# Kernel tuning notes

Hardware: AMD Instinct MI355X
Metric: run time of the kernel (lower is better)

Reference implementation:

```python
import jax, jax.numpy as jnp
import numpy as np

NHID = 512
T_K, T_Q, B = 256, 128, 8


def setup_inputs() -> dict:
    key = jax.random.key(0)
    k1, k2, k3, k4, k5 = jax.random.split(key, 5)
    query = jax.random.normal(k1, (T_Q, B, NHID), dtype=jnp.float32)
    c_key = jax.random.normal(k2, (T_K, B, NHID), dtype=jnp.float32)
    mask = jax.random.randint(k3, (T_K, B), 0, 2).astype(bool)
    # att_mlp params: Linear(2*nhid, nhid) -> Tanh -> Linear(nhid, 1)
    # stored as [in, out] so y = x @ W + b (torch Linear weight transposed)
    W1 = jax.random.normal(k4, (2 * NHID, NHID), dtype=jnp.float32) / np.sqrt(2 * NHID)
    b1 = jnp.zeros((NHID,), dtype=jnp.float32)
    W2 = jax.random.normal(k5, (NHID, 1), dtype=jnp.float32) / np.sqrt(NHID)
    b2 = jnp.zeros((1,), dtype=jnp.float32)
    return {"query": query, "c_key": c_key, "mask": mask,
            "W1": W1, "b1": b1, "W2": W2, "b2": b2}


def reference(query, c_key, mask, W1, b1, W2, b2):
    H = query.shape[-1]
    # cat([k_expand, q_expand], -1) @ W1 == k @ W1[:H] + q @ W1[H:]
    # (avoids materializing the [T_k, T_q, B, 2H] concat the torch code builds)
    k_proj = jnp.einsum('kbh,hd->kbd', c_key, W1[:H])   # [T_k, B, H]
    q_proj = jnp.einsum('qbh,hd->qbd', query, W1[H:])   # [T_q, B, H]
    h = jnp.tanh(k_proj[:, None, :, :] + q_proj[None, :, :, :] + b1)  # [T_k, T_q, B, H]
    att_score = jnp.einsum('kqbh,ho->kqb', h, W2) + b2[0]             # [T_k, T_q, B]
    att_score = jnp.where(mask[:, None, :], -jnp.inf, att_score)
    att_prob = jax.nn.softmax(att_score, axis=0)                      # softmax over keys
    # c_val defaults to c_key in the original forward
    ant_vec = jnp.einsum('kqb,kbh->qbh', att_prob, c_key)             # [T_q, B, H]
    return ant_vec, att_prob
```

## Files before the change

### kernel.cpp

```cpp
#include <hip/hip_runtime.h>
#include <math.h>

#define NHID 512
#define T_K  256
#define T_Q  128
#define BB   8

constexpr float C2L2E = 2.8853900817779268f;
constexpr float L2E   = 1.4426950408889634f;

__device__ __forceinline__ float fexp2(float x) { return __builtin_amdgcn_exp2f(x); }
__device__ __forceinline__ float frcp(float x)  { return __builtin_amdgcn_rcpf(x); }

typedef __attribute__((ext_vector_type(8))) short bf16x8;
typedef __attribute__((ext_vector_type(4))) float f32x4;

__device__ __forceinline__ unsigned short f2bf(float x) {
    unsigned u = __builtin_bit_cast(unsigned, x);
    unsigned r = (u + 0x7FFFu + ((u >> 16) & 1u)) >> 16;
    return (unsigned short)r;
}
__device__ __forceinline__ float bf2f(unsigned short h) {
    unsigned u = ((unsigned)h) << 16;
    return __builtin_bit_cast(float, u);
}

__global__ __launch_bounds__(256) void convert_w1_kernel(
    const float* __restrict__ W1,
    unsigned short* __restrict__ bt_hi, unsigned short* __restrict__ bt_lo)
{
    const int tb = blockIdx.x;
    const int kt = tb & 15;
    const int nt = tb >> 4;
    __shared__ float tile[64][65];
    const int t  = threadIdx.x;
    const int r  = t >> 2;
    const int c0 = (t & 3) * 16;
    const float* src = W1 + (size_t)(kt * 64 + r) * 512 + nt * 64 + c0;
    #pragma unroll
    for (int j = 0; j < 4; ++j) {
        const float4 v = *(const float4*)&src[j * 4];
        tile[r][c0 + j * 4 + 0] = v.x; tile[r][c0 + j * 4 + 1] = v.y;
        tile[r][c0 + j * 4 + 2] = v.z; tile[r][c0 + j * 4 + 3] = v.w;
    }
    __syncthreads();
    const size_t dst = (size_t)((kt >> 3) * 512 + nt * 64 + r) * 512
                     + (size_t)((kt & 7) * 64 + c0);
    #pragma unroll
    for (int j4 = 0; j4 < 4; ++j4) {
        ushort4 h, l;
        #pragma unroll
        for (int e = 0; e < 4; ++e) {
            const float x = tile[c0 + j4 * 4 + e][r];
            const unsigned short hb = f2bf(x);
            const unsigned short lb = f2bf(x - bf2f(hb));
            ((unsigned short*)&h)[e] = hb;
            ((unsigned short*)&l)[e] = lb;
        }
        *(ushort4*)&bt_hi[dst + j4 * 4] = h;
        *(ushort4*)&bt_lo[dst + j4 * 4] = l;
    }
}

__global__ __launch_bounds__(256) void proj_kernel(
    const float* __restrict__ qry, const float* __restrict__ ckey,
    const unsigned short* __restrict__ bt_hi, const unsigned short* __restrict__ bt_lo,
    const float* __restrict__ b1,
    float* __restrict__ ek, float* __restrict__ eq)
{
    const int row0 = blockIdx.x * 64;
    const int col0 = blockIdx.y * 64;
    const bool isK = row0 < 2048;
    const int bhalf = isK ? 0 : 512;

    __shared__ __align__(16) unsigned short As_h[64 * 64];
    __shared__ __align__(16) unsigned short As_l[64 * 64];
    __shared__ __align__(16) unsigned short Bs_h[64 * 64];
    __shared__ __align__(16) unsigned short Bs_l[64 * 64];

    const int t    = threadIdx.x;
    const int wave = t >> 6;
    const int lane = t & 63;
    const int wm = (wave & 1) * 32;
    const int wn = (wave >> 1) * 32;

    f32x4 acc[2][2] = {};

    const int sr = t >> 2;
    const int sc = (t & 3) * 16;
    const float* gA = (isK ? ckey + (size_t)(row0 + sr) * 512
                           : qry  + (size_t)(row0 - 2048 + sr) * 512) + sc;
    const unsigned short* gBh = bt_hi + (size_t)(bhalf + col0 + sr) * 512 + sc;
    const unsigned short* gBl = bt_lo + (size_t)(bhalf + col0 + sr) * 512 + sc;
    const int c0c = sc >> 3;
    const int sw0 = ((c0c + 0) ^ (sr & 7)) * 8;
    const int sw1 = ((c0c + 1) ^ (sr & 7)) * 8;

    const int quad = lane >> 4, fr = lane & 15;

    for (int k0 = 0; k0 < 512; k0 += 64) {
        __syncthreads();
        {
            float fa[16];
            *(float4*)&fa[0]  = *(const float4*)&gA[k0 + 0];
            *(float4*)&fa[4]  = *(const float4*)&gA[k0 + 4];
            *(float4*)&fa[8]  = *(const float4*)&gA[k0 + 8];
            *(float4*)&fa[12] = *(const float4*)&gA[k0 + 12];
            union { uint4 v; unsigned short s[8]; } h0, l0, h1, l1;
            #pragma unroll
            for (int e = 0; e < 8; ++e) {
                const unsigned short hb = f2bf(fa[e]);
                h0.s[e] = hb; l0.s[e] = f2bf(fa[e] - bf2f(hb));
            }
            #pragma unroll
            for (int e = 0; e < 8; ++e) {
                const unsigned short hb = f2bf(fa[8 + e]);
                h1.s[e] = hb; l1.s[e] = f2bf(fa[8 + e] - bf2f(hb));
            }
            *(uint4*)&As_h[sr * 64 + sw0] = h0.v; *(uint4*)&As_h[sr * 64 + sw1] = h1.v;
            *(uint4*)&As_l[sr * 64 + sw0] = l0.v; *(uint4*)&As_l[sr * 64 + sw1] = l1.v;
            uint4 v0, v1;
            v0 = *(const uint4*)&gBh[k0];     v1 = *(const uint4*)&gBh[k0 + 8];
            *(uint4*)&Bs_h[sr * 64 + sw0] = v0; *(uint4*)&Bs_h[sr * 64 + sw1] = v1;
            v0 = *(const uint4*)&gBl[k0];     v1 = *(const uint4*)&gBl[k0 + 8];
            *(uint4*)&Bs_l[sr * 64 + sw0] = v0; *(uint4*)&Bs_l[sr * 64 + sw1] = v1;
        }
        __syncthreads();
        #pragma unroll
        for (int ks = 0; ks < 2; ++ks) {
            const int cchunk = ks * 4 + quad;
            bf16x8 afh[2], afl[2], bfh[2], bfl[2];
            #pragma unroll
            for (int mt = 0; mt < 2; ++mt) {
                const int m = wm + mt * 16 + fr;
                afh[mt] = *(const bf16x8*)&As_h[m * 64 + ((cchunk ^ (m & 7)) * 8)];
                afl[mt] = *(const bf16x8*)&As_l[m * 64 + ((cchunk ^ (m & 7)) * 8)];
            }
            #pragma unroll
            for (int nt = 0; nt < 2; ++nt) {
                const int n = wn + nt * 16 + fr;
                bfh[nt] = *(const bf16x8*)&Bs_h[n * 64 + ((cchunk ^ (n & 7)) * 8)];
                bfl[nt] = *(const bf16x8*)&Bs_l[n * 64 + ((cchunk ^ (n & 7)) * 8)];
            }
            #pragma unroll
            for (int mt = 0; mt < 2; ++mt)
                #pragma unroll
                for (int nt = 0; nt < 2; ++nt) {
                    acc[mt][nt] = __builtin_amdgcn_mfma_f32_16x16x32_bf16(afh[mt], bfh[nt], acc[mt][nt], 0, 0, 0);
                    acc[mt][nt] = __builtin_amdgcn_mfma_f32_16x16x32_bf16(afh[mt], bfl[nt], acc[mt][nt], 0, 0, 0);
                    acc[mt][nt] = __builtin_amdgcn_mfma_f32_16x16x32_bf16(afl[mt], bfh[nt], acc[mt][nt], 0, 0, 0);
                }
        }
    }

    #pragma unroll
    for (int nt = 0; nt < 2; ++nt) {
        const int colg = col0 + wn + nt * 16 + fr;
        const float b1v = b1[colg];
        #pragma unroll
        for (int mt = 0; mt < 2; ++mt) {
            #pragma unroll
            for (int i = 0; i < 4; ++i) {
                const int rowg = row0 + wm + mt * 16 + quad * 4 + i;
                const float v = acc[mt][nt][i];
                if (isK) ek[(size_t)rowg * 512 + colg] = fexp2((v + b1v) * C2L2E);
                else     eq[(size_t)(rowg - 2048) * 512 + colg] = fexp2(v * C2L2E);
            }
        }
    }
}

__global__ __launch_bounds__(256) void score_kernel(
    const float* __restrict__ ek, const float* __restrict__ eq,
    const float* __restrict__ W2, const float* __restrict__ b2,
    const int* __restrict__ mask, float* __restrict__ score)
{
    const int t    = threadIdx.x;
    const int wave = __builtin_amdgcn_readfirstlane(t >> 6);
    const int lane = t & 63;
    const int kk = lane >> 1;
    const int p  = lane & 1;
    const int k0 = blockIdx.x * 32;
    const int q0 = blockIdx.y * 8;
    const int b  = blockIdx.z;

    __shared__ float kb[2][32][66];
    __shared__ float qb[2][8][66];
    __shared__ float w2s[512];

    *(float2*)&w2s[t * 2] = *(const float2*)&W2[t * 2];

    const float4 wA = *(const float4*)&W2[lane * 4];
    const float4 wB = *(const float4*)&W2[256 + lane * 4];
    float s2 = wA.x + wA.y + wA.z + wA.w + wB.x + wB.y + wB.z + wB.w;
    #pragma unroll
    for (int m = 32; m; m >>= 1) s2 += __shfl_xor(s2, m, 64);
    const float base = s2 + b2[0];

    const int srk = t >> 3;
    const int sck = (t & 7) * 8;
    const float* ek_src = ek + ((size_t)(k0 + srk) * 8 + b) * 512 + sck;
    const int srq = t >> 5;
    const int scq = (t & 31) * 2;
    const float* eq_src = eq + ((size_t)(q0 + srq) * 8 + b) * 512 + scq;

    float4 pk0 = *(const float4*)&ek_src[0];
    float4 pk1 = *(const float4*)&ek_src[4];
    float2 pq0 = *(const float2*)&eq_src[0];

    *(float2*)&kb[0][srk][sck + 0] = {pk0.x, pk0.y};
    *(float2*)&kb[0][srk][sck + 2] = {pk0.z, pk0.w};
    *(float2*)&kb[0][srk][sck + 4] = {pk1.x, pk1.y};
    *(float2*)&kb[0][srk][sck + 6] = {pk1.z, pk1.w};
    *(float2*)&qb[0][srq][scq] = pq0;
    __syncthreads();

    float racc[2] = {0.f, 0.f};

    for (int chunk = 0; chunk < 8; ++chunk) {
        const int buf = chunk & 1;
        const int hc = chunk * 64;
        if (chunk < 7) {
            pk0 = *(const float4*)&ek_src[hc + 64];
            pk1 = *(const float4*)&ek_src[hc + 68];
            pq0 = *(const float2*)&eq_src[hc + 64];
        }
        #pragma unroll
        for (int s = 0; s < 16; ++s) {
            const float2 e01 = *(const float2*)&kb[buf][kk][4 * s + 2 * p];
            const float2 w01 = *(const float2*)&w2s[hc + 4 * s + 2 * p];
            const float wsum = w01.x + w01.y;
            #pragma unroll
            for (int qi = 0; qi < 2; ++qi) {
                const float2 g01 = *(const float2*)&qb[buf][wave * 2 + qi][4 * s + 2 * p];
                const float t0 = e01.x * g01.x;
                const float t1 = e01.y * g01.y;
                const float a   = fmaf(t0, t1, t0);
                const float bb1 = t1 + 1.0f;
                const float den = a + bb1;
                const float num = fmaf(w01.x, t1, fmaf(w01.y, t0, wsum));
                racc[qi] = fmaf(num, frcp(den), racc[qi]);
            }
        }
        __syncthreads();
        if (chunk < 7) {
            const int nb = buf ^ 1;
            *(float2*)&kb[nb][srk][sck + 0] = {pk0.x, pk0.y};
            *(float2*)&kb[nb][srk][sck + 2] = {pk0.z, pk0.w};
            *(float2*)&kb[nb][srk][sck + 4] = {pk1.x, pk1.y};
            *(float2*)&kb[nb][srk][sck + 6] = {pk1.z, pk1.w};
            *(float2*)&qb[nb][srq][scq] = pq0;
        }
        __syncthreads();
    }

    const int kglob = k0 + kk;
    const int msk = mask[kglob * 8 + b];
    #pragma unroll
    for (int qi = 0; qi < 2; ++qi) {
        float r = racc[qi] + __shfl_xor(racc[qi], 1, 64);
        float sc = base - 2.0f * r;
        if (msk) sc = -INFINITY;
        if (p == 0)
            score[((size_t)(q0 + wave * 2 + qi) * 8 + b) * 256 + kglob] = sc;
    }
}

__global__ __launch_bounds__(256) void smav_kernel(
    const float* __restrict__ score, const float* __restrict__ ckey,
    float* __restrict__ prob_out, float* __restrict__ out_ant)
{
    const int qt = blockIdx.x;
    const int b  = blockIdx.y;
    const int t  = threadIdx.x;
    const int wave = __builtin_amdgcn_readfirstlane(t >> 6);
    const int lane = t & 63;
    const int q  = qt * 4 + wave;
    const int qb_idx = q * 8 + b;

    __shared__ float p_lds[4][256];
    __shared__ float pacc[4][4][512];

    float4 s4 = *(const float4*)&score[(size_t)qb_idx * 256 + lane * 4];
    float m = fmaxf(fmaxf(s4.x, s4.y), fmaxf(s4.z, s4.w));
    #pragma unroll
    for (int d = 32; d; d >>= 1) m = fmaxf(m, __shfl_xor(m, d, 64));

    float4 pv;
    pv.x = fexp2((s4.x - m) * L2E);
    pv.y = fexp2((s4.y - m) * L2E);
    pv.z = fexp2((s4.z - m) * L2E);
    pv.w = fexp2((s4.w - m) * L2E);
    float sum = pv.x + pv.y + pv.z + pv.w;
    #pragma unroll
    for (int d = 32; d; d >>= 1) sum += __shfl_xor(sum, d, 64);
    const float inv = frcp(sum);
    pv.x *= inv; pv.y *= inv; pv.z *= inv; pv.w *= inv;

    *(float4*)&p_lds[wave][lane * 4] = pv;
    const int kbase = lane * 4;
    prob_out[(size_t)(kbase + 0) * 1024 + qb_idx] = pv.x;
    prob_out[(size_t)(kbase + 1) * 1024 + qb_idx] = pv.y;
    prob_out[(size_t)(kbase + 2) * 1024 + qb_idx] = pv.z;
    prob_out[(size_t)(kbase + 3) * 1024 + qb_idx] = pv.w;
    __syncthreads();

    const int h0 = lane * 8;
    float4 accL[4] = {}, accH[4] = {};
    const int kstart = wave * 64;
    #pragma unroll 4
    for (int ki = 0; ki < 64; ++ki) {
        const int k = kstart + ki;
        const float* ckp = &ckey[((size_t)k * 8 + b) * 512 + h0];
        const float4 c0 = *(const float4*)&ckp[0];
        const float4 c1 = *(const float4*)&ckp[4];
        #pragma unroll
        for (int qi = 0; qi < 4; ++qi) {
            const float pq = p_lds[qi][k];
            accL[qi].x = fmaf(pq, c0.x, accL[qi].x);
            accL[qi].y = fmaf(pq, c0.y, accL[qi].y);
            accL[qi].z = fmaf(pq, c0.z, accL[qi].z);
            accL[qi].w = fmaf(pq, c0.w, accL[qi].w);
            accH[qi].x = fmaf(pq, c1.x, accH[qi].x);
            accH[qi].y = fmaf(pq, c1.y, accH[qi].y);
            accH[qi].z = fmaf(pq, c1.z, accH[qi].z);
            accH[qi].w = fmaf(pq, c1.w, accH[qi].w);
        }
    }
    #pragma unroll
    for (int qi = 0; qi < 4; ++qi) {
        *(float4*)&pacc[wave][qi][h0 + 0] = accL[qi];
        *(float4*)&pacc[wave][qi][h0 + 4] = accH[qi];
    }
    __syncthreads();

    const int h2 = t * 2;
    #pragma unroll
    for (int qi = 0; qi < 4; ++qi) {
        float2 r0 = *(const float2*)&pacc[0][qi][h2];
        float2 r1 = *(const float2*)&pacc[1][qi][h2];
        float2 r2 = *(const float2*)&pacc[2][qi][h2];
        float2 r3 = *(const float2*)&pacc[3][qi][h2];
        float2 r;
        r.x = (r0.x + r1.x) + (r2.x + r3.x);
        r.y = (r0.y + r1.y) + (r2.y + r3.y);
        *(float2*)&out_ant[((size_t)(qt * 4 + qi) * 8 + b) * 512 + h2] = r;
    }
}

extern "C" void kernel_launch(void* const* d_in, const int* in_sizes, int n_in,
                              void* d_out, int out_size, void* d_ws, size_t ws_size,
                              hipStream_t stream)
{
    const float* qry  = (const float*)d_in[0];
    const float* ckey = (const float*)d_in[1];
    const int*   mask = (const int*)d_in[2];
    const float* W1   = (const float*)d_in[3];
    const float* b1   = (const float*)d_in[4];
    const float* W2   = (const float*)d_in[5];
    const float* b2   = (const float*)d_in[6];

    float* out_ant  = (float*)d_out;
    float* out_prob = (float*)d_out + T_Q * BB * NHID;

    float* ws = (float*)d_ws;
    float* ws_ek = ws;
    float* ws_eq = ws + 1048576;
    unsigned short* bt_hi = (unsigned short*)(ws + 1572864);
    unsigned short* bt_lo = (unsigned short*)(ws + 1835008);
    float* ws_sc = ws + 2097152;

    convert_w1_kernel<<<dim3(128), 256, 0, stream>>>(W1, bt_hi, bt_lo);
    proj_kernel<<<dim3(48, 8), 256, 0, stream>>>(qry, ckey, bt_hi, bt_lo, b1, ws_ek, ws_eq);
    score_kernel<<<dim3(8, 16, 8), 256, 0, stream>>>(ws_ek, ws_eq, W2, b2, mask, ws_sc);
    smav_kernel<<<dim3(32, 8), 256, 0, stream>>>(ws_sc, ckey, out_prob, out_ant);
}
```

Measured before the change: 124.4 us.

## Fuse four stage kernels into one persistent cooperative kernel with grid syncs

Replaces the four separate launches (W1 conversion, projection GEMM, score, softmax+AV) with a single cooperative persistent kernel. The stages run as grid-strided loops separated by grid.sync(), with a union of shared-memory layouts. The aim is to remove the per-launch overhead and tail gaps between the small kernels. In exchange it adds grid-wide barrier costs, caps occupancy at up to 512 blocks, and leaves some stages with fewer blocks than work units. The old four-kernel path stays as a fallback if the cooperative launch fails.

```diff
diff --git a/kernel.cpp b/kernel.cpp
--- a/kernel.cpp
+++ b/kernel.cpp
@@ -1,5 +1,8 @@
 #include <hip/hip_runtime.h>
+#include <hip/hip_cooperative_groups.h>
 #include <math.h>
+
+namespace cg = cooperative_groups;
 
 #define NHID 512
 #define T_K  256
@@ -23,6 +26,318 @@
 __device__ __forceinline__ float bf2f(unsigned short h) {
     unsigned u = ((unsigned)h) << 16;
     return __builtin_bit_cast(float, u);
+}
+
+union MegaShared {
+    struct { unsigned short Ah[4096], Al[4096], Bh[4096], Bl[4096]; } pj;
+    struct { float tile[64][65]; } cv;
+    struct { float kb[2][32][66]; float qb[2][8][66]; float w2s[512]; } sc;
+    struct { float p[4][256]; float pacc[4][4][512]; } sv;
+};
+
+__global__ __launch_bounds__(256, 2) void mega_kernel(
+    const float* __restrict__ qry, const float* __restrict__ ckey,
+    const int* __restrict__ mask, const float* __restrict__ W1,
+    const float* __restrict__ b1, const float* __restrict__ W2,
+    const float* __restrict__ b2,
+    unsigned short* __restrict__ bt_hi, unsigned short* __restrict__ bt_lo,
+    float* __restrict__ ek, float* __restrict__ eq, float* __restrict__ sc_ws,
+    float* __restrict__ out_prob, float* __restrict__ out_ant)
+{
+    cg::grid_group grid = cg::this_grid();
+    __shared__ MegaShared sh;
+    const int t    = threadIdx.x;
+    const int lane = t & 63;
+    const int wave = __builtin_amdgcn_readfirstlane(t >> 6);
+    const unsigned nb = gridDim.x;
+
+    for (unsigned u = blockIdx.x; u < 128; u += nb) {
+        const int kt = u & 15, nt = u >> 4;
+        const int r  = t >> 2;
+        const int c0 = (t & 3) * 16;
+        const float* src = W1 + (size_t)(kt * 64 + r) * 512 + nt * 64 + c0;
+        #pragma unroll
+        for (int j = 0; j < 4; ++j) {
+            const float4 v = *(const float4*)&src[j * 4];
+            sh.cv.tile[r][c0 + j * 4 + 0] = v.x; sh.cv.tile[r][c0 + j * 4 + 1] = v.y;
+            sh.cv.tile[r][c0 + j * 4 + 2] = v.z; sh.cv.tile[r][c0 + j * 4 + 3] = v.w;
+        }
+        __syncthreads();
+        const size_t dst = (size_t)((kt >> 3) * 512 + nt * 64 + r) * 512
+                         + (size_t)((kt & 7) * 64 + c0);
+        #pragma unroll
+        for (int j4 = 0; j4 < 4; ++j4) {
+            ushort4 h, l;
+            #pragma unroll
+            for (int e = 0; e < 4; ++e) {
+                const float x = sh.cv.tile[c0 + j4 * 4 + e][r];
+                const unsigned short hb = f2bf(x);
+                ((unsigned short*)&h)[e] = hb;
+                ((unsigned short*)&l)[e] = f2bf(x - bf2f(hb));
+            }
+            *(ushort4*)&bt_hi[dst + j4 * 4] = h;
+            *(ushort4*)&bt_lo[dst + j4 * 4] = l;
+        }
+        __syncthreads();
+    }
+    grid.sync();
+
+    for (unsigned u = blockIdx.x; u < 384; u += nb) {
+        const int row0 = (int)(u % 48) * 64;
+        const int col0 = (int)(u / 48) * 64;
+        const bool isK = row0 < 2048;
+        const int bhalf = isK ? 0 : 512;
+
+        const int wm = (wave & 1) * 32;
+        const int wn = (wave >> 1) * 32;
+        f32x4 acc[2][2] = {};
+
+        const int sr = t >> 2;
+        const int sc = (t & 3) * 16;
+        const float* gA = (isK ? ckey + (size_t)(row0 + sr) * 512
+                               : qry  + (size_t)(row0 - 2048 + sr) * 512) + sc;
+        const unsigned short* gBh = bt_hi + (size_t)(bhalf + col0 + sr) * 512 + sc;
+        const unsigned short* gBl = bt_lo + (size_t)(bhalf + col0 + sr) * 512 + sc;
+        const int c0c = sc >> 3;
+        const int sw0 = ((c0c + 0) ^ (sr & 7)) * 8;
+        const int sw1 = ((c0c + 1) ^ (sr & 7)) * 8;
+        const int quad = lane >> 4, fr = lane & 15;
+
+        for (int k0 = 0; k0 < 512; k0 += 64) {
+            __syncthreads();
+            {
+                float fa[16];
+                *(float4*)&fa[0]  = *(const float4*)&gA[k0 + 0];
+                *(float4*)&fa[4]  = *(const float4*)&gA[k0 + 4];
+                *(float4*)&fa[8]  = *(const float4*)&gA[k0 + 8];
+                *(float4*)&fa[12] = *(const float4*)&gA[k0 + 12];
+                union { uint4 v; unsigned short s[8]; } h0, l0, h1, l1;
+                #pragma unroll
+                for (int e = 0; e < 8; ++e) {
+                    const unsigned short hb = f2bf(fa[e]);
+                    h0.s[e] = hb; l0.s[e] = f2bf(fa[e] - bf2f(hb));
+                }
+                #pragma unroll
+                for (int e = 0; e < 8; ++e) {
+                    const unsigned short hb = f2bf(fa[8 + e]);
+                    h1.s[e] = hb; l1.s[e] = f2bf(fa[8 + e] - bf2f(hb));
+                }
+                *(uint4*)&sh.pj.Ah[sr * 64 + sw0] = h0.v; *(uint4*)&sh.pj.Ah[sr * 64 + sw1] = h1.v;
+                *(uint4*)&sh.pj.Al[sr * 64 + sw0] = l0.v; *(uint4*)&sh.pj.Al[sr * 64 + sw1] = l1.v;
+                uint4 v0, v1;
+                v0 = *(const uint4*)&gBh[k0];     v1 = *(const uint4*)&gBh[k0 + 8];
+                *(uint4*)&sh.pj.Bh[sr * 64 + sw0] = v0; *(uint4*)&sh.pj.Bh[sr * 64 + sw1] = v1;
+                v0 = *(const uint4*)&gBl[k0];     v1 = *(const uint4*)&gBl[k0 + 8];
+                *(uint4*)&sh.pj.Bl[sr * 64 + sw0] = v0; *(uint4*)&sh.pj.Bl[sr * 64 + sw1] = v1;
+            }
+            __syncthreads();
+            #pragma unroll
+            for (int ks = 0; ks < 2; ++ks) {
+                const int cchunk = ks * 4 + quad;
+                bf16x8 afh[2], afl[2], bfh[2], bfl[2];
+                #pragma unroll
+                for (int mt = 0; mt < 2; ++mt) {
+                    const int m = wm + mt * 16 + fr;
+                    afh[mt] = *(const bf16x8*)&sh.pj.Ah[m * 64 + ((cchunk ^ (m & 7)) * 8)];
+                    afl[mt] = *(const bf16x8*)&sh.pj.Al[m * 64 + ((cchunk ^ (m & 7)) * 8)];
+                }
+                #pragma unroll
+                for (int nt = 0; nt < 2; ++nt) {
+                    const int n = wn + nt * 16 + fr;
+                    bfh[nt] = *(const bf16x8*)&sh.pj.Bh[n * 64 + ((cchunk ^ (n & 7)) * 8)];
+                    bfl[nt] = *(const bf16x8*)&sh.pj.Bl[n * 64 + ((cchunk ^ (n & 7)) * 8)];
+                }
+                #pragma unroll
+                for (int mt = 0; mt < 2; ++mt)
+                    #pragma unroll
+                    for (int nt = 0; nt < 2; ++nt) {
+                        acc[mt][nt] = __builtin_amdgcn_mfma_f32_16x16x32_bf16(afh[mt], bfh[nt], acc[mt][nt], 0, 0, 0);
+                        acc[mt][nt] = __builtin_amdgcn_mfma_f32_16x16x32_bf16(afh[mt], bfl[nt], acc[mt][nt], 0, 0, 0);
+                        acc[mt][nt] = __builtin_amdgcn_mfma_f32_16x16x32_bf16(afl[mt], bfh[nt], acc[mt][nt], 0, 0, 0);
+                    }
+            }
+        }
+        #pragma unroll
+        for (int nt = 0; nt < 2; ++nt) {
+            const int colg = col0 + wn + nt * 16 + fr;
+            const float b1v = b1[colg];
+            #pragma unroll
+            for (int mt = 0; mt < 2; ++mt) {
+                #pragma unroll
+                for (int i = 0; i < 4; ++i) {
+                    const int rowg = row0 + wm + mt * 16 + quad * 4 + i;
+                    const float v = acc[mt][nt][i];
+                    if (isK) ek[(size_t)rowg * 512 + colg] = fexp2((v + b1v) * C2L2E);
+                    else     eq[(size_t)(rowg - 2048) * 512 + colg] = fexp2(v * C2L2E);
+                }
+            }
+        }
+        __syncthreads();
+    }
+    grid.sync();
+
+    {
+        const float4 wA = *(const float4*)&W2[lane * 4];
+        const float4 wB = *(const float4*)&W2[256 + lane * 4];
+        float s2 = wA.x + wA.y + wA.z + wA.w + wB.x + wB.y + wB.z + wB.w;
+        #pragma unroll
+        for (int m = 32; m; m >>= 1) s2 += __shfl_xor(s2, m, 64);
+        const float base = s2 + b2[0];
+
+        *(float2*)&sh.sc.w2s[t * 2] = *(const float2*)&W2[t * 2];
+        __syncthreads();
+
+        const int kk = lane >> 1;
+        const int p  = lane & 1;
+        const int srk = t >> 3;
+        const int sck = (t & 7) * 8;
+        const int srq = t >> 5;
+        const int scq = (t & 31) * 2;
+
+        for (unsigned u = blockIdx.x; u < 1024; u += nb) {
+            const int k0 = (int)(u & 7) * 32;
+            const int q0 = (int)((u >> 3) & 15) * 8;
+            const int b  = (int)(u >> 7);
+
+            const float* ek_src = ek + ((size_t)(k0 + srk) * 8 + b) * 512 + sck;
+            const float* eq_src = eq + ((size_t)(q0 + srq) * 8 + b) * 512 + scq;
+
+            float4 pk0 = *(const float4*)&ek_src[0];
+            float4 pk1 = *(const float4*)&ek_src[4];
+            float2 pq0 = *(const float2*)&eq_src[0];
+
+            *(float2*)&sh.sc.kb[0][srk][sck + 0] = {pk0.x, pk0.y};
+            *(float2*)&sh.sc.kb[0][srk][sck + 2] = {pk0.z, pk0.w};
+            *(float2*)&sh.sc.kb[0][srk][sck + 4] = {pk1.x, pk1.y};
+            *(float2*)&sh.sc.kb[0][srk][sck + 6] = {pk1.z, pk1.w};
+            *(float2*)&sh.sc.qb[0][srq][scq] = pq0;
+            __syncthreads();
+
+            float racc[2] = {0.f, 0.f};
+            for (int chunk = 0; chunk < 8; ++chunk) {
+                const int buf = chunk & 1;
+                const int hc = chunk * 64;
+                if (chunk < 7) {
+                    pk0 = *(const float4*)&ek_src[hc + 64];
+                    pk1 = *(const float4*)&ek_src[hc + 68];
+                    pq0 = *(const float2*)&eq_src[hc + 64];
+                }
+                #pragma unroll
+                for (int s = 0; s < 16; ++s) {
+                    const float2 e01 = *(const float2*)&sh.sc.kb[buf][kk][4 * s + 2 * p];
+                    const float2 w01 = *(const float2*)&sh.sc.w2s[hc + 4 * s + 2 * p];
+                    const float wsum = w01.x + w01.y;
+                    #pragma unroll
+                    for (int qi = 0; qi < 2; ++qi) {
+                        const float2 g01 = *(const float2*)&sh.sc.qb[buf][wave * 2 + qi][4 * s + 2 * p];
+                        const float t0 = e01.x * g01.x;
+                        const float t1 = e01.y * g01.y;
+                        const float a   = fmaf(t0, t1, t0);
+                        const float bb1 = t1 + 1.0f;
+                        const float den = a + bb1;
+                        const float num = fmaf(w01.x, t1, fmaf(w01.y, t0, wsum));
+                        racc[qi] = fmaf(num, frcp(den), racc[qi]);
+                    }
+                }
+                __syncthreads();
+                if (chunk < 7) {
+                    const int nxt = buf ^ 1;
+                    *(float2*)&sh.sc.kb[nxt][srk][sck + 0] = {pk0.x, pk0.y};
+                    *(float2*)&sh.sc.kb[nxt][srk][sck + 2] = {pk0.z, pk0.w};
+                    *(float2*)&sh.sc.kb[nxt][srk][sck + 4] = {pk1.x, pk1.y};
+                    *(float2*)&sh.sc.kb[nxt][srk][sck + 6] = {pk1.z, pk1.w};
+                    *(float2*)&sh.sc.qb[nxt][srq][scq] = pq0;
+                }
+                __syncthreads();
+            }
+
+            const int kglob = k0 + kk;
+            const int msk = mask[kglob * 8 + b];
+            #pragma unroll
+            for (int qi = 0; qi < 2; ++qi) {
+                float r = racc[qi] + __shfl_xor(racc[qi], 1, 64);
+                float scv = base - 2.0f * r;
+                if (msk) scv = -INFINITY;
+                if (p == 0)
+                    sc_ws[((size_t)(q0 + wave * 2 + qi) * 8 + b) * 256 + kglob] = scv;
+            }
+        }
+    }
+    grid.sync();
+
+    for (unsigned u = blockIdx.x; u < 256; u += nb) {
+        const int qt = (int)(u >> 3);
+        const int b  = (int)(u & 7);
+        const int q  = qt * 4 + wave;
+        const int qb_idx = q * 8 + b;
+
+        float4 s4 = *(const float4*)&sc_ws[(size_t)qb_idx * 256 + lane * 4];
+        float m = fmaxf(fmaxf(s4.x, s4.y), fmaxf(s4.z, s4.w));
+        #pragma unroll
+        for (int d = 32; d; d >>= 1) m = fmaxf(m, __shfl_xor(m, d, 64));
+
+        float4 pv;
+        pv.x = fexp2((s4.x - m) * L2E);
+        pv.y = fexp2((s4.y - m) * L2E);
+        pv.z = fexp2((s4.z - m) * L2E);
+        pv.w = fexp2((s4.w - m) * L2E);
+        float sum = pv.x + pv.y + pv.z + pv.w;
+        #pragma unroll
+        for (int d = 32; d; d >>= 1) sum += __shfl_xor(sum, d, 64);
+        const float inv = frcp(sum);
+        pv.x *= inv; pv.y *= inv; pv.z *= inv; pv.w *= inv;
+
+        *(float4*)&sh.sv.p[wave][lane * 4] = pv;
+        const int kbase = lane * 4;
+        out_prob[(size_t)(kbase + 0) * 1024 + qb_idx] = pv.x;
+        out_prob[(size_t)(kbase + 1) * 1024 + qb_idx] = pv.y;
+        out_prob[(size_t)(kbase + 2) * 1024 + qb_idx] = pv.z;
+        out_prob[(size_t)(kbase + 3) * 1024 + qb_idx] = pv.w;
+        __syncthreads();
+
+        const int h0 = lane * 8;
+        float4 accL[4] = {}, accH[4] = {};
+        const int kstart = wave * 64;
+        #pragma unroll 4
+        for (int ki = 0; ki < 64; ++ki) {
+            const int k = kstart + ki;
+            const float* ckp = &ckey[((size_t)k * 8 + b) * 512 + h0];
+            const float4 c0 = *(const float4*)&ckp[0];
+            const float4 c1 = *(const float4*)&ckp[4];
+            #pragma unroll
+            for (int qi = 0; qi < 4; ++qi) {
+                const float pq = sh.sv.p[qi][k];
+                accL[qi].x = fmaf(pq, c0.x, accL[qi].x);
+                accL[qi].y = fmaf(pq, c0.y, accL[qi].y);
+                accL[qi].z = fmaf(pq, c0.z, accL[qi].z);
+                accL[qi].w = fmaf(pq, c0.w, accL[qi].w);
+                accH[qi].x = fmaf(pq, c1.x, accH[qi].x);
+                accH[qi].y = fmaf(pq, c1.y, accH[qi].y);
+                accH[qi].z = fmaf(pq, c1.z, accH[qi].z);
+                accH[qi].w = fmaf(pq, c1.w, accH[qi].w);
+            }
+        }
+        #pragma unroll
+        for (int qi = 0; qi < 4; ++qi) {
+            *(float4*)&sh.sv.pacc[wave][qi][h0 + 0] = accL[qi];
+            *(float4*)&sh.sv.pacc[wave][qi][h0 + 4] = accH[qi];
+        }
+        __syncthreads();
+
+        const int h2 = t * 2;
+        #pragma unroll
+        for (int qi = 0; qi < 4; ++qi) {
+            float2 r0 = *(const float2*)&sh.sv.pacc[0][qi][h2];
+            float2 r1 = *(const float2*)&sh.sv.pacc[1][qi][h2];
+            float2 r2 = *(const float2*)&sh.sv.pacc[2][qi][h2];
+            float2 r3 = *(const float2*)&sh.sv.pacc[3][qi][h2];
+            float2 r;
+            r.x = (r0.x + r1.x) + (r2.x + r3.x);
+            r.y = (r0.y + r1.y) + (r2.y + r3.y);
+            *(float2*)&out_ant[((size_t)(qt * 4 + qi) * 8 + b) * 512 + h2] = r;
+        }
+        __syncthreads();
+    }
 }
 
 __global__ __launch_bounds__(256) void convert_w1_kernel(
@@ -53,9 +368,8 @@
         for (int e = 0; e < 4; ++e) {
             const float x = tile[c0 + j4 * 4 + e][r];
             const unsigned short hb = f2bf(x);
-            const unsigned short lb = f2bf(x - bf2f(hb));
             ((unsigned short*)&h)[e] = hb;
-            ((unsigned short*)&l)[e] = lb;
+            ((unsigned short*)&l)[e] = f2bf(x - bf2f(hb));
         }
         *(ushort4*)&bt_hi[dst + j4 * 4] = h;
         *(ushort4*)&bt_lo[dst + j4 * 4] = l;
@@ -244,12 +558,12 @@
         }
         __syncthreads();
         if (chunk < 7) {
-            const int nb = buf ^ 1;
-            *(float2*)&kb[nb][srk][sck + 0] = {pk0.x, pk0.y};
-            *(float2*)&kb[nb][srk][sck + 2] = {pk0.z, pk0.w};
-            *(float2*)&kb[nb][srk][sck + 4] = {pk1.x, pk1.y};
-            *(float2*)&kb[nb][srk][sck + 6] = {pk1.z, pk1.w};
-            *(float2*)&qb[nb][srq][scq] = pq0;
+            const int nxt = buf ^ 1;
+            *(float2*)&kb[nxt][srk][sck + 0] = {pk0.x, pk0.y};
+            *(float2*)&kb[nxt][srk][sck + 2] = {pk0.z, pk0.w};
+            *(float2*)&kb[nxt][srk][sck + 4] = {pk1.x, pk1.y};
+            *(float2*)&kb[nxt][srk][sck + 6] = {pk1.z, pk1.w};
+            *(float2*)&qb[nxt][srq][scq] = pq0;
         }
         __syncthreads();
     }
@@ -370,8 +684,25 @@
     unsigned short* bt_lo = (unsigned short*)(ws + 1835008);
     float* ws_sc = ws + 2097152;
 
-    convert_w1_kernel<<<dim3(128), 256, 0, stream>>>(W1, bt_hi, bt_lo);
-    proj_kernel<<<dim3(48, 8), 256, 0, stream>>>(qry, ckey, bt_hi, bt_lo, b1, ws_ek, ws_eq);
-    score_kernel<<<dim3(8, 16, 8), 256, 0, stream>>>(ws_ek, ws_eq, W2, b2, mask, ws_sc);
-    smav_kernel<<<dim3(32, 8), 256, 0, stream>>>(ws_sc, ckey, out_prob, out_ant);
+    int maxB = 0;
+    (void)hipOccupancyMaxActiveBlocksPerMultiprocessor(&maxB, mega_kernel, 256, 0);
+    int nb = (maxB > 0) ? maxB * 256 : 0;
+    if (nb > 512) nb = 512;
+
+    hipError_t st = hipErrorUnknown;
+    if (nb > 0) {
+        void* args[] = {
+            (void*)&qry, (void*)&ckey, (void*)&mask, (void*)&W1, (void*)&b1,
+            (void*)&W2, (void*)&b2, (void*)&bt_hi, (void*)&bt_lo,
+            (void*)&ws_ek, (void*)&ws_eq, (void*)&ws_sc,
+            (void*)&out_prob, (void*)&out_ant };
+        st = hipLaunchCooperativeKernel(reinterpret_cast<void*>(mega_kernel),
+                                        dim3(nb), dim3(256), args, 0, stream);
+    }
+    if (st != hipSuccess) {
+        convert_w1_kernel<<<dim3(128), 256, 0, stream>>>(W1, bt_hi, bt_lo);
+        proj_kernel<<<dim3(48, 8), 256, 0, stream>>>(qry, ckey, bt_hi, bt_lo, b1, ws_ek, ws_eq);
+        score_kernel<<<dim3(8, 16, 8), 256, 0, stream>>>(ws_ek, ws_eq, W2, b2, mask, ws_sc);
+        smav_kernel<<<dim3(32, 8), 256, 0, stream>>>(ws_sc, ckey, out_prob, out_ant);
+    }
 }
```

Result: slower. 270.3 us (+117.3%).

## Fuse score computation with softmax and attention-weighted sum into one kernel

Applied to the files above, without the earlier changes.

Merges the score kernel and the softmax/AV kernel into a single kernel where each block owns two queries and one batch across all 256 keys. Each thread handles one key, streams its ek row through padded LDS in 16-wide chunks, and reads eq and W2 directly from global memory, which should be broadcast through cache. The per-element math is rewritten as a product of (1+t) terms. This removes the intermediate score buffer and one launch, but it cuts the grid from 1024 blocks to 512. The AV part now reuses each ckey load across only 2 queries instead of 4, so ckey traffic doubles.

```diff
diff --git a/kernel.cpp b/kernel.cpp
--- a/kernel.cpp
+++ b/kernel.cpp
@@ -53,9 +53,8 @@
         for (int e = 0; e < 4; ++e) {
             const float x = tile[c0 + j4 * 4 + e][r];
             const unsigned short hb = f2bf(x);
-            const unsigned short lb = f2bf(x - bf2f(hb));
             ((unsigned short*)&h)[e] = hb;
-            ((unsigned short*)&l)[e] = lb;
+            ((unsigned short*)&l)[e] = f2bf(x - bf2f(hb));
         }
         *(ushort4*)&bt_hi[dst + j4 * 4] = h;
         *(ushort4*)&bt_lo[dst + j4 * 4] = l;
@@ -170,25 +169,22 @@
     }
 }
 
-__global__ __launch_bounds__(256) void score_kernel(
+__global__ __launch_bounds__(256) void scoreav_kernel(
     const float* __restrict__ ek, const float* __restrict__ eq,
     const float* __restrict__ W2, const float* __restrict__ b2,
-    const int* __restrict__ mask, float* __restrict__ score)
+    const int* __restrict__ mask, const float* __restrict__ ckey,
+    float* __restrict__ prob_out, float* __restrict__ out_ant)
 {
     const int t    = threadIdx.x;
+    const int lane = t & 63;
     const int wave = __builtin_amdgcn_readfirstlane(t >> 6);
-    const int lane = t & 63;
-    const int kk = lane >> 1;
-    const int p  = lane & 1;
-    const int k0 = blockIdx.x * 32;
-    const int q0 = blockIdx.y * 8;
-    const int b  = blockIdx.z;
-
-    __shared__ float kb[2][32][66];
-    __shared__ float qb[2][8][66];
-    __shared__ float w2s[512];
-
-    *(float2*)&w2s[t * 2] = *(const float2*)&W2[t * 2];
+    const int q0   = blockIdx.x * 2;
+    const int b    = blockIdx.y;
+    const int myk  = wave * 64 + lane;
+
+    __shared__ float eks[2][256 * 19];
+    __shared__ float ps[2][256];
+    __shared__ float pacc[4][2][512];
 
     const float4 wA = *(const float4*)&W2[lane * 4];
     const float4 wB = *(const float4*)&W2[256 + lane * 4];
@@ -197,154 +193,142 @@
     for (int m = 32; m; m >>= 1) s2 += __shfl_xor(s2, m, 64);
     const float base = s2 + b2[0];
 
-    const int srk = t >> 3;
-    const int sck = (t & 7) * 8;
-    const float* ek_src = ek + ((size_t)(k0 + srk) * 8 + b) * 512 + sck;
-    const int srq = t >> 5;
-    const int scq = (t & 31) * 2;
-    const float* eq_src = eq + ((size_t)(q0 + srq) * 8 + b) * 512 + scq;
-
-    float4 pk0 = *(const float4*)&ek_src[0];
-    float4 pk1 = *(const float4*)&ek_src[4];
-    float2 pq0 = *(const float2*)&eq_src[0];
-
-    *(float2*)&kb[0][srk][sck + 0] = {pk0.x, pk0.y};
-    *(float2*)&kb[0][srk][sck + 2] = {pk0.z, pk0.w};
-    *(float2*)&kb[0][srk][sck + 4] = {pk1.x, pk1.y};
-    *(float2*)&kb[0][srk][sck + 6] = {pk1.z, pk1.w};
-    *(float2*)&qb[0][srq][scq] = pq0;
-    __syncthreads();
-
-    float racc[2] = {0.f, 0.f};
-
-    for (int chunk = 0; chunk < 8; ++chunk) {
+    const float* __restrict__ eqr0 = eq + (size_t)(q0 * 8 + b) * 512;
+    const float* __restrict__ eqr1 = eq + (size_t)((q0 + 1) * 8 + b) * 512;
+
+    const float* __restrict__ ekg = ek + ((size_t)t * 8 + b) * 512;
+
+    {
+        float fa[16];
+        *(float4*)&fa[0]  = *(const float4*)&ekg[0];
+        *(float4*)&fa[4]  = *(const float4*)&ekg[4];
+        *(float4*)&fa[8]  = *(const float4*)&ekg[8];
+        *(float4*)&fa[12] = *(const float4*)&ekg[12];
+        #pragma unroll
+        for (int j = 0; j < 16; ++j) eks[0][t * 19 + j] = fa[j];
+    }
+    __syncthreads();
+
+    float racc0 = 0.0f, racc1 = 0.0f;
+
+    for (int chunk = 0; chunk < 32; ++chunk) {
         const int buf = chunk & 1;
-        const int hc = chunk * 64;
-        if (chunk < 7) {
-            pk0 = *(const float4*)&ek_src[hc + 64];
-            pk1 = *(const float4*)&ek_src[hc + 68];
-            pq0 = *(const float2*)&eq_src[hc + 64];
-        }
-        #pragma unroll
-        for (int s = 0; s < 16; ++s) {
-            const float2 e01 = *(const float2*)&kb[buf][kk][4 * s + 2 * p];
-            const float2 w01 = *(const float2*)&w2s[hc + 4 * s + 2 * p];
-            const float wsum = w01.x + w01.y;
-            #pragma unroll
-            for (int qi = 0; qi < 2; ++qi) {
-                const float2 g01 = *(const float2*)&qb[buf][wave * 2 + qi][4 * s + 2 * p];
-                const float t0 = e01.x * g01.x;
-                const float t1 = e01.y * g01.y;
-                const float a   = fmaf(t0, t1, t0);
-                const float bb1 = t1 + 1.0f;
-                const float den = a + bb1;
-                const float num = fmaf(w01.x, t1, fmaf(w01.y, t0, wsum));
-                racc[qi] = fmaf(num, frcp(den), racc[qi]);
+        const int hc  = chunk * 16;
+        float nf[16];
+        if (chunk < 31) {
+            *(float4*)&nf[0]  = *(const float4*)&ekg[hc + 16];
+            *(float4*)&nf[4]  = *(const float4*)&ekg[hc + 20];
+            *(float4*)&nf[8]  = *(const float4*)&ekg[hc + 24];
+            *(float4*)&nf[12] = *(const float4*)&ekg[hc + 28];
+        }
+        #pragma unroll
+        for (int s = 0; s < 8; ++s) {
+            const float ek0 = eks[buf][myk * 19 + 2 * s + 0];
+            const float ek1 = eks[buf][myk * 19 + 2 * s + 1];
+            const int h = hc + 2 * s;
+            const float w0 = W2[h], w1 = W2[h + 1];
+            const float e0 = eqr0[h], e1 = eqr0[h + 1];
+            const float f0 = eqr1[h], f1 = eqr1[h + 1];
+            {
+                const float t0 = ek0 * e0, t1 = ek1 * e1;
+                const float a0 = t0 + 1.0f, a1 = t1 + 1.0f;
+                const float den = a0 * a1;
+                const float num = fmaf(w0, a1, w1 * a0);
+                racc0 = fmaf(num, frcp(den), racc0);
+            }
+            {
+                const float t0 = ek0 * f0, t1 = ek1 * f1;
+                const float a0 = t0 + 1.0f, a1 = t1 + 1.0f;
+                const float den = a0 * a1;
+                const float num = fmaf(w0, a1, w1 * a0);
+                racc1 = fmaf(num, frcp(den), racc1);
             }
         }
         __syncthreads();
-        if (chunk < 7) {
+        if (chunk < 31) {
             const int nb = buf ^ 1;
-            *(float2*)&kb[nb][srk][sck + 0] = {pk0.x, pk0.y};
-            *(float2*)&kb[nb][srk][sck + 2] = {pk0.z, pk0.w};
-            *(float2*)&kb[nb][srk][sck + 4] = {pk1.x, pk1.y};
-            *(float2*)&kb[nb][srk][sck + 6] = {pk1.z, pk1.w};
-            *(float2*)&qb[nb][srq][scq] = pq0;
+            #pragma unroll
+            for (int j = 0; j < 16; ++j) eks[nb][t * 19 + j] = nf[j];
         }
         __syncthreads();
     }
 
-    const int kglob = k0 + kk;
-    const int msk = mask[kglob * 8 + b];
-    #pragma unroll
-    for (int qi = 0; qi < 2; ++qi) {
-        float r = racc[qi] + __shfl_xor(racc[qi], 1, 64);
-        float sc = base - 2.0f * r;
-        if (msk) sc = -INFINITY;
-        if (p == 0)
-            score[((size_t)(q0 + wave * 2 + qi) * 8 + b) * 256 + kglob] = sc;
-    }
-}
-
-__global__ __launch_bounds__(256) void smav_kernel(
-    const float* __restrict__ score, const float* __restrict__ ckey,
-    float* __restrict__ prob_out, float* __restrict__ out_ant)
-{
-    const int qt = blockIdx.x;
-    const int b  = blockIdx.y;
-    const int t  = threadIdx.x;
-    const int wave = __builtin_amdgcn_readfirstlane(t >> 6);
-    const int lane = t & 63;
-    const int q  = qt * 4 + wave;
-    const int qb_idx = q * 8 + b;
-
-    __shared__ float p_lds[4][256];
-    __shared__ float pacc[4][4][512];
-
-    float4 s4 = *(const float4*)&score[(size_t)qb_idx * 256 + lane * 4];
-    float m = fmaxf(fmaxf(s4.x, s4.y), fmaxf(s4.z, s4.w));
-    #pragma unroll
-    for (int d = 32; d; d >>= 1) m = fmaxf(m, __shfl_xor(m, d, 64));
-
-    float4 pv;
-    pv.x = fexp2((s4.x - m) * L2E);
-    pv.y = fexp2((s4.y - m) * L2E);
-    pv.z = fexp2((s4.z - m) * L2E);
-    pv.w = fexp2((s4.w - m) * L2E);
-    float sum = pv.x + pv.y + pv.z + pv.w;
-    #pragma unroll
-    for (int d = 32; d; d >>= 1) sum += __shfl_xor(sum, d, 64);
-    const float inv = frcp(sum);
-    pv.x *= inv; pv.y *= inv; pv.z *= inv; pv.w *= inv;
-
-    *(float4*)&p_lds[wave][lane * 4] = pv;
-    const int kbase = lane * 4;
-    prob_out[(size_t)(kbase + 0) * 1024 + qb_idx] = pv.x;
-    prob_out[(size_t)(kbase + 1) * 1024 + qb_idx] = pv.y;
-    prob_out[(size_t)(kbase + 2) * 1024 + qb_idx] = pv.z;
-    prob_out[(size_t)(kbase + 3) * 1024 + qb_idx] = pv.w;
-    __syncthreads();
-
-    const int h0 = lane * 8;
-    float4 accL[4] = {}, accH[4] = {};
-    const int kstart = wave * 64;
-    #pragma unroll 4
-    for (int ki = 0; ki < 64; ++ki) {
-        const int k = kstart + ki;
-        const float* ckp = &ckey[((size_t)k * 8 + b) * 512 + h0];
-        const float4 c0 = *(const float4*)&ckp[0];
-        const float4 c1 = *(const float4*)&ckp[4];
-        #pragma unroll
-        for (int qi = 0; qi < 4; ++qi) {
-            const float pq = p_lds[qi][k];
-            accL[qi].x = fmaf(pq, c0.x, accL[qi].x);
-            accL[qi].y = fmaf(pq, c0.y, accL[qi].y);
-            accL[qi].z = fmaf(pq, c0.z, accL[qi].z);
-            accL[qi].w = fmaf(pq, c0.w, accL[qi].w);
-            accH[qi].x = fmaf(pq, c1.x, accH[qi].x);
-            accH[qi].y = fmaf(pq, c1.y, accH[qi].y);
-            accH[qi].z = fmaf(pq, c1.z, accH[qi].z);
-            accH[qi].w = fmaf(pq, c1.w, accH[qi].w);
-        }
-    }
-    #pragma unroll
-    for (int qi = 0; qi < 4; ++qi) {
-        *(float4*)&pacc[wave][qi][h0 + 0] = accL[qi];
-        *(float4*)&pacc[wave][qi][h0 + 4] = accH[qi];
-    }
-    __syncthreads();
-
-    const int h2 = t * 2;
-    #pragma unroll
-    for (int qi = 0; qi < 4; ++qi) {
-        float2 r0 = *(const float2*)&pacc[0][qi][h2];
-        float2 r1 = *(const float2*)&pacc[1][qi][h2];
-        float2 r2 = *(const float2*)&pacc[2][qi][h2];
-        float2 r3 = *(const float2*)&pacc[3][qi][h2];
-        float2 r;
-        r.x = (r0.x + r1.x) + (r2.x + r3.x);
-        r.y = (r0.y + r1.y) + (r2.y + r3.y);
-        *(float2*)&out_ant[((size_t)(qt * 4 + qi) * 8 + b) * 512 + h2] = r;
+    {
+        const int msk = mask[myk * 8 + b];
+        float s0 = base - 2.0f * racc0;
+        float s1 = base - 2.0f * racc1;
+        if (msk) { s0 = -INFINITY; s1 = -INFINITY; }
+        ps[0][myk] = s0;
+        ps[1][myk] = s1;
+    }
+    __syncthreads();
+
+    if (wave < 2) {
+        float4 sv = *(const float4*)&ps[wave][lane * 4];
+        float m = fmaxf(fmaxf(sv.x, sv.y), fmaxf(sv.z, sv.w));
+        #pragma unroll
+        for (int d = 32; d; d >>= 1) m = fmaxf(m, __shfl_xor(m, d, 64));
+        float4 pv;
+        pv.x = fexp2((sv.x - m) * L2E);
+        pv.y = fexp2((sv.y - m) * L2E);
+        pv.z = fexp2((sv.z - m) * L2E);
+        pv.w = fexp2((sv.w - m) * L2E);
+        float sum = pv.x + pv.y + pv.z + pv.w;
+        #pragma unroll
+        for (int d = 32; d; d >>= 1) sum += __shfl_xor(sum, d, 64);
+        const float inv = frcp(sum);
+        pv.x *= inv; pv.y *= inv; pv.z *= inv; pv.w *= inv;
+        *(float4*)&ps[wave][lane * 4] = pv;
+        const int qb_idx = (q0 + wave) * 8 + b;
+        const int kbase = lane * 4;
+        prob_out[(size_t)(kbase + 0) * 1024 + qb_idx] = pv.x;
+        prob_out[(size_t)(kbase + 1) * 1024 + qb_idx] = pv.y;
+        prob_out[(size_t)(kbase + 2) * 1024 + qb_idx] = pv.z;
+        prob_out[(size_t)(kbase + 3) * 1024 + qb_idx] = pv.w;
+    }
+    __syncthreads();
+
+    {
+        const int h0 = lane * 8;
+        float4 aL0 = {}, aH0 = {}, aL1 = {}, aH1 = {};
+        const int kstart = wave * 64;
+        #pragma unroll 4
+        for (int ki = 0; ki < 64; ++ki) {
+            const int k = kstart + ki;
+            const float* ckp = &ckey[((size_t)k * 8 + b) * 512 + h0];
+            const float4 c0 = *(const float4*)&ckp[0];
+            const float4 c1 = *(const float4*)&ckp[4];
+            const float p0 = ps[0][k];
+            const float p1 = ps[1][k];
+            aL0.x = fmaf(p0, c0.x, aL0.x); aL0.y = fmaf(p0, c0.y, aL0.y);
+            aL0.z = fmaf(p0, c0.z, aL0.z); aL0.w = fmaf(p0, c0.w, aL0.w);
+            aH0.x = fmaf(p0, c1.x, aH0.x); aH0.y = fmaf(p0, c1.y, aH0.y);
+            aH0.z = fmaf(p0, c1.z, aH0.z); aH0.w = fmaf(p0, c1.w, aH0.w);
+            aL1.x = fmaf(p1, c0.x, aL1.x); aL1.y = fmaf(p1, c0.y, aL1.y);
+            aL1.z = fmaf(p1, c0.z, aL1.z); aL1.w = fmaf(p1, c0.w, aL1.w);
+            aH1.x = fmaf(p1, c1.x, aH1.x); aH1.y = fmaf(p1, c1.y, aH1.y);
+            aH1.z = fmaf(p1, c1.z, aH1.z); aH1.w = fmaf(p1, c1.w, aH1.w);
+        }
+        *(float4*)&pacc[wave][0][h0 + 0] = aL0;
+        *(float4*)&pacc[wave][0][h0 + 4] = aH0;
+        *(float4*)&pacc[wave][1][h0 + 0] = aL1;
+        *(float4*)&pacc[wave][1][h0 + 4] = aH1;
+    }
+    __syncthreads();
+
+    {
+        const int h2 = t * 2;
+        #pragma unroll
+        for (int qi = 0; qi < 2; ++qi) {
+            float2 r0 = *(const float2*)&pacc[0][qi][h2];
+            float2 r1 = *(const float2*)&pacc[1][qi][h2];
+            float2 r2 = *(const float2*)&pacc[2][qi][h2];
+            float2 r3 = *(const float2*)&pacc[3][qi][h2];
+            float2 r;
+            r.x = (r0.x + r1.x) + (r2.x + r3.x);
+            r.y = (r0.y + r1.y) + (r2.y + r3.y);
+            *(float2*)&out_ant[((size_t)(q0 + qi) * 8 + b) * 512 + h2] = r;
+        }
     }
 }
 
@@ -368,10 +352,9 @@
     float* ws_eq = ws + 1048576;
     unsigned short* bt_hi = (unsigned short*)(ws + 1572864);
     unsigned short* bt_lo = (unsigned short*)(ws + 1835008);
-    float* ws_sc = ws + 2097152;
 
     convert_w1_kernel<<<dim3(128), 256, 0, stream>>>(W1, bt_hi, bt_lo);
     proj_kernel<<<dim3(48, 8), 256, 0, stream>>>(qry, ckey, bt_hi, bt_lo, b1, ws_ek, ws_eq);
-    score_kernel<<<dim3(8, 16, 8), 256, 0, stream>>>(ws_ek, ws_eq, W2, b2, mask, ws_sc);
-    smav_kernel<<<dim3(32, 8), 256, 0, stream>>>(ws_sc, ckey, out_prob, out_ant);
-}
+    scoreav_kernel<<<dim3(64, 8), 256, 0, stream>>>(ws_ek, ws_eq, W2, b2, mask, ckey,
+                                                    out_prob, out_ant);
+}
```

After: 126.3 us. No clear change (+1.5%).
